# Optimization experiments

Hardware: AMD Instinct MI355X
Metric: run time of the kernel (lower is better)

Reference implementation:

```python
import jax, jax.numpy as jnp
import numpy as np

N = 4096
TAU = 0.2          # args.tau relaxation temperature
EPS = 1e-10        # numerical guard for logit of clamped probs


def setup_inputs() -> dict:
    key = jax.random.key(0)
    k1, k2, k3 = jax.random.split(key, 3)
    r = jax.random.uniform(k1, (N, N))
    ori_adj = jnp.where(r < 0.005, -1.0, jnp.where(r < 0.01, 1.0, 0.0)).astype(jnp.float32)
    # nn.init.uniform_(change_links_prob, 0.0, 0.001)
    change_links_prob = jax.random.uniform(k2, (N, N), minval=0.0, maxval=0.001, dtype=jnp.float32)
    # uniform noise for the RelaxedBernoulli logistic reparameterization
    u = jax.random.uniform(k3, (N, N), minval=1e-6, maxval=1.0 - 1e-6, dtype=jnp.float32)
    return {"ori_adj": ori_adj, "change_links_prob": change_links_prob, "u": u}


def reference(ori_adj, change_links_prob, u):
    # --- get_modified_adj: RelaxedBernoulliStraightThrough(tau, clamp(p,0,1)).rsample() ---
    p = jnp.clip(change_links_prob, EPS, 1.0 - EPS)      # torch.clamp(p, 0, 1) + logit guard
    logits = jnp.log(p) - jnp.log1p(-p)
    noise = jnp.log(u) - jnp.log1p(-u)                   # logistic noise
    soft = jax.nn.sigmoid((logits + noise) / TAU)        # relaxed sample
    hard = jnp.round(soft)                               # quantized sample
    change_prob = soft + jax.lax.stop_gradient(hard - soft)  # straight-through
    mod_adj = ori_adj + change_prob * (-2.0 * ori_adj)   # ori_adj * (1 - 2*b)

    # --- balance_degree_directed(mod_adj) ---
    # torch.diag(matrix) returns the diagonal VECTOR, broadcast-subtracted per row (faithful).
    A = mod_adj + mod_adj.T - jnp.diag(mod_adj)
    A_abs = jnp.abs(A)
    tr3 = jnp.einsum('ij,jk,ki->', A, A, A)              # trace(A @ A @ A)
    tr3_abs = jnp.einsum('ij,jk,ki->', A_abs, A_abs, A_abs)
    balance = 0.5 * (1.0 + tr3 / tr3_abs)
    return mod_adj, balance
```

## Files before the change

kernel.cpp:

```cpp
#include <hip/hip_runtime.h>
#include <hip/hip_bf16.h>
#include <cstdint>
#include <cstddef>

#define N 4096
#define NN ((size_t)N * (size_t)N)

typedef int   int4v   __attribute__((ext_vector_type(4)));
typedef float float4v __attribute__((ext_vector_type(4)));

__device__ inline void async16(const void* g, void* lds) {
    __builtin_amdgcn_global_load_lds(
        (const __attribute__((address_space(1))) void*)g,
        (__attribute__((address_space(3))) void*)lds, 16, 0, 0);
}

__global__ void mod_kernel(const float* __restrict__ ori,
                           const float* __restrict__ clp,
                           const float* __restrict__ u,
                           float* __restrict__ out) {
    size_t i = ((size_t)blockIdx.x * blockDim.x + threadIdx.x) * 4;
    const float4v p4 = *(const float4v*)(clp + i);
    const float4v u4 = *(const float4v*)(u + i);
    const float4v o4 = *(const float4v*)(ori + i);
    float4v r;
    #pragma unroll
    for (int c = 0; c < 4; ++c) {
        float hard = (p4[c] + u4[c] >= 1.0f) ? 1.0f : 0.0f;
        r[c] = fmaf(hard, -2.0f * o4[c], o4[c]);
    }
    *(float4v*)(out + i) = r;
}

__global__ void diag_kernel(const float* __restrict__ mod,
                            float* __restrict__ diag,
                            double* __restrict__ accs) {
    int j = blockIdx.x * blockDim.x + threadIdx.x;
    if (j < N) diag[j] = mod[(size_t)j * N + j];
    if (blockIdx.x == 0 && threadIdx.x < 2) accs[threadIdx.x] = 0.0;
}

__global__ void build_A8(const float* __restrict__ mod,
                         const float* __restrict__ diag,
                         signed char* __restrict__ A,
                         signed char* __restrict__ AT,
                         signed char* __restrict__ Aa,
                         signed char* __restrict__ ATa) {
    __shared__ float tji[32][33];
    __shared__ signed char cv[32][36];
    const int bi = blockIdx.x * 32;
    const int bj = blockIdx.y * 32;
    const int tx = threadIdx.x;
    const int ty = threadIdx.y;
    {
        const float4 v = *(const float4*)&mod[(size_t)(bj + ty) * N + bi + tx * 4];
        tji[ty][tx * 4 + 0] = v.x; tji[ty][tx * 4 + 1] = v.y;
        tji[ty][tx * 4 + 2] = v.z; tji[ty][tx * 4 + 3] = v.w;
    }
    __syncthreads();
    const float4 mv = *(const float4*)&mod[(size_t)(bi + ty) * N + bj + tx * 4];
    float m4[4] = {mv.x, mv.y, mv.z, mv.w};
    int pkA = 0, pkAa = 0;
    #pragma unroll
    for (int k = 0; k < 4; ++k) {
        int jl = tx * 4 + k;
        float a = m4[k] + tji[jl][ty] - diag[bj + jl];
        int ai = (int)a;
        cv[ty][jl] = (signed char)ai;
        int au = ai < 0 ? -ai : ai;
        pkA  |= (ai & 255) << (8 * k);
        pkAa |= (au & 255) << (8 * k);
    }
    *(int*)&A [(size_t)(bi + ty) * N + bj + tx * 4] = pkA;
    *(int*)&Aa[(size_t)(bi + ty) * N + bj + tx * 4] = pkAa;
    __syncthreads();
    int pkT = 0, pkTa = 0;
    #pragma unroll
    for (int k = 0; k < 4; ++k) {
        int il = tx * 4 + k;
        int v = cv[il][ty];
        int va = v < 0 ? -v : v;
        pkT  |= (v  & 255) << (8 * k);
        pkTa |= (va & 255) << (8 * k);
    }
    *(int*)&AT [(size_t)(bj + ty) * N + bi + tx * 4] = pkT;
    *(int*)&ATa[(size_t)(bj + ty) * N + bi + tx * 4] = pkTa;
}

#define BK 64
#define NT (N / BK)
#define BUFSZ 32768

__global__ __launch_bounds__(512, 2) void gemm_trace_i8(
        const signed char* __restrict__ Ag,
        const signed char* __restrict__ ATg,
        const signed char* __restrict__ Aag,
        const signed char* __restrict__ ATag,
        double* __restrict__ accs) {
    __shared__ __align__(16) signed char lds[4 * BUFSZ];
    __shared__ int red[8];
    const int z = blockIdx.z;
    const signed char* Asrc = z ? Aag  : Ag;
    const signed char* Bsrc = z ? ATag : ATg;
    const int i0 = blockIdx.y * 256;
    const int k0 = blockIdx.x * 256;
    const int t = threadIdx.x;
    const int lane = t & 63;
    const int wave = t >> 6;
    const int wm = wave >> 2;
    const int wn = wave & 3;
    const int quad = lane >> 4;
    const int col  = lane & 15;

    const int c1 = t;
    const int r1 = c1 >> 2;
    const int r2 = r1 + 128;
    const int s1 = (((c1 & 3) ^ ((r1 >> 1) & 3)) << 4);
    const int s2 = (((c1 & 3) ^ ((r2 >> 1) & 3)) << 4);
    const signed char* gA1 = Asrc + (size_t)(i0 + r1) * N + s1;
    const signed char* gA2 = Asrc + (size_t)(i0 + r2) * N + s2;
    const signed char* gB1 = Bsrc + (size_t)(k0 + r1) * N + s1;
    const signed char* gB2 = Bsrc + (size_t)(k0 + r2) * N + s2;
    const int ldsA1 = (wave * 64) * 16;
    const int ldsA2 = 8192  + (wave * 64) * 16;
    const int ldsB1 = 16384 + (wave * 64) * 16;
    const int ldsB2 = 24576 + (wave * 64) * 16;
    const int fsw = ((quad ^ ((col >> 1) & 3)) << 4);

    int4v acc[8][4];
    #pragma unroll
    for (int a = 0; a < 8; ++a)
        #pragma unroll
        for (int b = 0; b < 4; ++b)
            acc[a][b] = (int4v){0, 0, 0, 0};

    for (int p = 0; p < 3; ++p) {
        const int pb = p * BUFSZ;
        const size_t go = (size_t)p * BK;
        async16(gA1 + go, lds + pb + ldsA1);
        async16(gA2 + go, lds + pb + ldsA2);
        async16(gB1 + go, lds + pb + ldsB1);
        async16(gB2 + go, lds + pb + ldsB2);
    }
    asm volatile("s_waitcnt vmcnt(8)" ::: "memory");
    __builtin_amdgcn_s_barrier();
    __builtin_amdgcn_sched_barrier(0);

    for (int j = 0; j < NT; ++j) {
        const int buf = (j & 3) * BUFSZ;
        const signed char* Ab = lds + buf;
        const signed char* Bb = lds + buf + 16384;
        const int pre = j + 3;
        const size_t go = (size_t)pre * BK;
        const int pb = (pre & 3) * BUFSZ;
        int4v af0[4], af1[4], bf[4];
        #pragma unroll
        for (int tr = 0; tr < 4; ++tr)
            af0[tr] = *(const int4v*)(Ab + ((wm * 128 + tr * 16 + col) << 6) + fsw);
        #pragma unroll
        for (int tc = 0; tc < 4; ++tc)
            bf[tc] = *(const int4v*)(Bb + ((wn * 64 + tc * 16 + col) << 6) + fsw);
        #pragma unroll
        for (int tr = 0; tr < 4; ++tr)
            af1[tr] = *(const int4v*)(Ab + ((wm * 128 + 64 + tr * 16 + col) << 6) + fsw);
        if (pre < NT) {
            async16(gA1 + go, lds + pb + ldsA1);
            async16(gA2 + go, lds + pb + ldsA2);
            async16(gB1 + go, lds + pb + ldsB1);
            async16(gB2 + go, lds + pb + ldsB2);
        }
        asm volatile("s_waitcnt lgkmcnt(4)" ::: "memory");
        __builtin_amdgcn_sched_barrier(0);
        __builtin_amdgcn_s_setprio(1);
        #pragma unroll
        for (int tr = 0; tr < 4; ++tr)
            #pragma unroll
            for (int tc = 0; tc < 4; ++tc)
                acc[tr][tc] = __builtin_amdgcn_mfma_i32_16x16x64_i8(af0[tr], bf[tc], acc[tr][tc], 0, 0, 0);
        __builtin_amdgcn_s_setprio(0);
        asm volatile("s_waitcnt lgkmcnt(0)" ::: "memory");
        __builtin_amdgcn_sched_barrier(0);
        __builtin_amdgcn_s_setprio(1);
        #pragma unroll
        for (int tr = 0; tr < 4; ++tr)
            #pragma unroll
            for (int tc = 0; tc < 4; ++tc)
                acc[4 + tr][tc] = __builtin_amdgcn_mfma_i32_16x16x64_i8(af1[tr], bf[tc], acc[4 + tr][tc], 0, 0, 0);
        __builtin_amdgcn_s_setprio(0);
        if (j < NT - 3)       { asm volatile("s_waitcnt vmcnt(8)" ::: "memory"); }
        else if (j == NT - 3) { asm volatile("s_waitcnt vmcnt(4)" ::: "memory"); }
        else if (j == NT - 2) { asm volatile("s_waitcnt vmcnt(0)" ::: "memory"); }
        __builtin_amdgcn_s_barrier();
        __builtin_amdgcn_sched_barrier(0);
    }

    int part = 0;
    #pragma unroll
    for (int mr = 0; mr < 8; ++mr) {
        const int ib = i0 + wm * 128 + mr * 16 + quad * 4;
        #pragma unroll
        for (int tc = 0; tc < 4; ++tc) {
            const int kk = k0 + wn * 64 + tc * 16 + col;
            const int mv = *(const int*)&Asrc[(size_t)kk * N + ib];
            #pragma unroll
            for (int r = 0; r < 4; ++r)
                part += acc[mr][tc][r] * (int)(signed char)(mv >> (8 * r));
        }
    }
    #pragma unroll
    for (int off = 32; off > 0; off >>= 1)
        part += __shfl_down(part, off, 64);
    if (lane == 0) red[wave] = part;
    __syncthreads();
    if (t == 0) {
        int tot = 0;
        #pragma unroll
        for (int w = 0; w < 8; ++w) tot += red[w];
        atomicAdd(&accs[z], (double)tot);
    }
}

__global__ void finalize_kernel(const double* __restrict__ accs, float* __restrict__ out) {
    out[NN] = (float)(0.5 * (1.0 + accs[0] / accs[1]));
}

extern "C" void kernel_launch(void* const* d_in, const int* in_sizes, int n_in,
                              void* d_out, int out_size, void* d_ws, size_t ws_size,
                              hipStream_t stream) {
    const float* ori = (const float*)d_in[0];
    const float* clp = (const float*)d_in[1];
    const float* u   = (const float*)d_in[2];
    float* out = (float*)d_out;
    char* ws = (char*)d_ws;
    signed char* A8   = (signed char*)ws;
    signed char* AT8  = (signed char*)(ws + NN);
    signed char* Aa8  = (signed char*)(ws + 2 * NN);
    signed char* ATa8 = (signed char*)(ws + 3 * NN);
    float*       diag = (float*)(ws + 4 * NN);
    double*      accs = (double*)(ws + 4 * NN + 4096 * 4);

    mod_kernel<<<dim3((unsigned)(NN / 1024)), 256, 0, stream>>>(ori, clp, u, out);
    diag_kernel<<<dim3(16), 256, 0, stream>>>(out, diag, accs);
    build_A8<<<dim3(N / 32, N / 32), dim3(8, 32), 0, stream>>>(out, diag, A8, AT8, Aa8, ATa8);
    gemm_trace_i8<<<dim3(N / 256, N / 256, 2), 512, 0, stream>>>(A8, AT8, Aa8, ATa8, accs);
    finalize_kernel<<<1, 1, 0, stream>>>(accs, out);
}
```

Before: 365.6 us.

## Fuse mod_adj computation, diagonal extraction, and int8 A build into one symmetric-tile kernel

Merges the elementwise mod_adj kernel, the diagonal kernel, and the int8 A/AT build into a single kernel. Each block handles an upper-triangular tile pair (I,J) and its mirror, recomputing mod values directly from the inputs, so the float mod_adj is no longer re-read from memory. The diagonal is recomputed locally for each block. This removes two launches and a full read of the float matrix, but half the blocks exit immediately and each active block does more work.

```diff
diff --git a/kernel.cpp b/kernel.cpp
--- a/kernel.cpp
+++ b/kernel.cpp
@@ -15,76 +15,96 @@
         (__attribute__((address_space(3))) void*)lds, 16, 0, 0);
 }
 
-__global__ void mod_kernel(const float* __restrict__ ori,
-                           const float* __restrict__ clp,
-                           const float* __restrict__ u,
-                           float* __restrict__ out) {
-    size_t i = ((size_t)blockIdx.x * blockDim.x + threadIdx.x) * 4;
-    const float4v p4 = *(const float4v*)(clp + i);
-    const float4v u4 = *(const float4v*)(u + i);
-    const float4v o4 = *(const float4v*)(ori + i);
-    float4v r;
-    #pragma unroll
-    for (int c = 0; c < 4; ++c) {
-        float hard = (p4[c] + u4[c] >= 1.0f) ? 1.0f : 0.0f;
-        r[c] = fmaf(hard, -2.0f * o4[c], o4[c]);
-    }
-    *(float4v*)(out + i) = r;
-}
-
-__global__ void diag_kernel(const float* __restrict__ mod,
-                            float* __restrict__ diag,
-                            double* __restrict__ accs) {
-    int j = blockIdx.x * blockDim.x + threadIdx.x;
-    if (j < N) diag[j] = mod[(size_t)j * N + j];
-    if (blockIdx.x == 0 && threadIdx.x < 2) accs[threadIdx.x] = 0.0;
-}
-
-__global__ void build_A8(const float* __restrict__ mod,
-                         const float* __restrict__ diag,
-                         signed char* __restrict__ A,
-                         signed char* __restrict__ AT,
-                         signed char* __restrict__ Aa,
-                         signed char* __restrict__ ATa) {
-    __shared__ float tji[32][33];
-    __shared__ signed char cv[32][36];
-    const int bi = blockIdx.x * 32;
-    const int bj = blockIdx.y * 32;
+__global__ void fused_mod_build(const float* __restrict__ ori,
+                                const float* __restrict__ clp,
+                                const float* __restrict__ uu,
+                                float* __restrict__ out,
+                                signed char* __restrict__ A,
+                                signed char* __restrict__ AT,
+                                signed char* __restrict__ Aa,
+                                signed char* __restrict__ ATa,
+                                double* __restrict__ accs) {
+    const int I = blockIdx.x, J = blockIdx.y;
+    if (I > J) return;
+    __shared__ float sm1[32][33];
+    __shared__ float sm2[32][33];
+    __shared__ float dI[32], dJ[32];
     const int tx = threadIdx.x;
     const int ty = threadIdx.y;
+    const int t = ty * 8 + tx;
+    const int bi = I * 32, bj = J * 32;
+    if (I == 0 && J == 0 && t < 2) accs[t] = 0.0;
+    if (t < 64) {
+        const int x = (t < 32) ? (bi + t) : (bj + (t - 32));
+        const size_t off = (size_t)x * N + x;
+        const float o = ori[off];
+        const float hard = (clp[off] + uu[off] >= 1.0f) ? 1.0f : 0.0f;
+        const float d = fmaf(hard, -2.0f * o, o);
+        if (t < 32) dI[t] = d; else dJ[t - 32] = d;
+    }
     {
-        const float4 v = *(const float4*)&mod[(size_t)(bj + ty) * N + bi + tx * 4];
-        tji[ty][tx * 4 + 0] = v.x; tji[ty][tx * 4 + 1] = v.y;
-        tji[ty][tx * 4 + 2] = v.z; tji[ty][tx * 4 + 3] = v.w;
+        const size_t off = (size_t)(bi + ty) * N + bj + tx * 4;
+        const float4v o4 = *(const float4v*)(ori + off);
+        const float4v p4 = *(const float4v*)(clp + off);
+        const float4v u4 = *(const float4v*)(uu + off);
+        float4v m;
+        #pragma unroll
+        for (int c = 0; c < 4; ++c) {
+            const float hard = (p4[c] + u4[c] >= 1.0f) ? 1.0f : 0.0f;
+            m[c] = fmaf(hard, -2.0f * o4[c], o4[c]);
+            sm1[ty][tx * 4 + c] = m[c];
+        }
+        *(float4v*)(out + off) = m;
+    }
+    {
+        const size_t off = (size_t)(bj + ty) * N + bi + tx * 4;
+        const float4v o4 = *(const float4v*)(ori + off);
+        const float4v p4 = *(const float4v*)(clp + off);
+        const float4v u4 = *(const float4v*)(uu + off);
+        float4v m;
+        #pragma unroll
+        for (int c = 0; c < 4; ++c) {
+            const float hard = (p4[c] + u4[c] >= 1.0f) ? 1.0f : 0.0f;
+            m[c] = fmaf(hard, -2.0f * o4[c], o4[c]);
+            sm2[ty][tx * 4 + c] = m[c];
+        }
+        if (I != J) *(float4v*)(out + off) = m;
     }
     __syncthreads();
-    const float4 mv = *(const float4*)&mod[(size_t)(bi + ty) * N + bj + tx * 4];
-    float m4[4] = {mv.x, mv.y, mv.z, mv.w};
-    int pkA = 0, pkAa = 0;
+    int pkA1 = 0, pkAa1 = 0, pkT1 = 0, pkTa1 = 0;
+    int pkA2 = 0, pkAa2 = 0, pkT2 = 0, pkTa2 = 0;
     #pragma unroll
     for (int k = 0; k < 4; ++k) {
-        int jl = tx * 4 + k;
-        float a = m4[k] + tji[jl][ty] - diag[bj + jl];
-        int ai = (int)a;
-        cv[ty][jl] = (signed char)ai;
-        int au = ai < 0 ? -ai : ai;
-        pkA  |= (ai & 255) << (8 * k);
-        pkAa |= (au & 255) << (8 * k);
-    }
-    *(int*)&A [(size_t)(bi + ty) * N + bj + tx * 4] = pkA;
-    *(int*)&Aa[(size_t)(bi + ty) * N + bj + tx * 4] = pkAa;
-    __syncthreads();
-    int pkT = 0, pkTa = 0;
-    #pragma unroll
-    for (int k = 0; k < 4; ++k) {
-        int il = tx * 4 + k;
-        int v = cv[il][ty];
-        int va = v < 0 ? -v : v;
-        pkT  |= (v  & 255) << (8 * k);
-        pkTa |= (va & 255) << (8 * k);
-    }
-    *(int*)&AT [(size_t)(bj + ty) * N + bi + tx * 4] = pkT;
-    *(int*)&ATa[(size_t)(bj + ty) * N + bi + tx * 4] = pkTa;
+        const int c = tx * 4 + k;
+        const float a1 = sm1[ty][c] + sm2[c][ty] - dJ[c];
+        const int v1 = (int)a1;  const int u1 = v1 < 0 ? -v1 : v1;
+        pkA1  |= (v1 & 255) << (8 * k);
+        pkAa1 |= (u1 & 255) << (8 * k);
+        const float t1 = sm1[c][ty] + sm2[ty][c] - dJ[ty];
+        const int w1 = (int)t1;  const int x1 = w1 < 0 ? -w1 : w1;
+        pkT1  |= (w1 & 255) << (8 * k);
+        pkTa1 |= (x1 & 255) << (8 * k);
+        const float a2 = sm2[ty][c] + sm1[c][ty] - dI[c];
+        const int v2 = (int)a2;  const int u2 = v2 < 0 ? -v2 : v2;
+        pkA2  |= (v2 & 255) << (8 * k);
+        pkAa2 |= (u2 & 255) << (8 * k);
+        const float t2 = sm2[c][ty] + sm1[ty][c] - dI[ty];
+        const int w2 = (int)t2;  const int x2 = w2 < 0 ? -w2 : w2;
+        pkT2  |= (w2 & 255) << (8 * k);
+        pkTa2 |= (x2 & 255) << (8 * k);
+    }
+    const size_t oIJ = (size_t)(bi + ty) * N + bj + tx * 4;
+    const size_t oJI = (size_t)(bj + ty) * N + bi + tx * 4;
+    *(int*)&A  [oIJ] = pkA1;
+    *(int*)&Aa [oIJ] = pkAa1;
+    *(int*)&AT [oJI] = pkT1;
+    *(int*)&ATa[oJI] = pkTa1;
+    if (I != J) {
+        *(int*)&A  [oJI] = pkA2;
+        *(int*)&Aa [oJI] = pkAa2;
+        *(int*)&AT [oIJ] = pkT2;
+        *(int*)&ATa[oIJ] = pkTa2;
+    }
 }
 
 #define BK 64
@@ -236,12 +256,10 @@
     signed char* AT8  = (signed char*)(ws + NN);
     signed char* Aa8  = (signed char*)(ws + 2 * NN);
     signed char* ATa8 = (signed char*)(ws + 3 * NN);
-    float*       diag = (float*)(ws + 4 * NN);
-    double*      accs = (double*)(ws + 4 * NN + 4096 * 4);
-
-    mod_kernel<<<dim3((unsigned)(NN / 1024)), 256, 0, stream>>>(ori, clp, u, out);
-    diag_kernel<<<dim3(16), 256, 0, stream>>>(out, diag, accs);
-    build_A8<<<dim3(N / 32, N / 32), dim3(8, 32), 0, stream>>>(out, diag, A8, AT8, Aa8, ATa8);
+    double*      accs = (double*)(ws + 4 * NN);
+
+    fused_mod_build<<<dim3(128, 128), dim3(8, 32), 0, stream>>>(
+        ori, clp, u, out, A8, AT8, Aa8, ATa8, accs);
     gemm_trace_i8<<<dim3(N / 256, N / 256, 2), 512, 0, stream>>>(A8, AT8, Aa8, ATa8, accs);
     finalize_kernel<<<1, 1, 0, stream>>>(accs, out);
 }
```

Result: slower. 381.0 us (+4.2%).
